# Optimization experiments

Measured on AMD Instinct MI355X. Metric: run time of the kernel, lower is better.

Reference implementation:

```python
import jax, jax.numpy as jnp
import numpy as np

N_NODES = 100000

def gcn_conv(x, row, col, w, W, b, n):
    # PyG GCNConv with edge weights: add self-loops, symmetric normalization.
    loop = jnp.arange(n)
    r = jnp.concatenate([row, loop])
    c = jnp.concatenate([col, loop])
    ew = jnp.concatenate([w, jnp.ones((n,), dtype=x.dtype)])
    deg = jax.ops.segment_sum(ew, c, num_segments=n)          # [N]
    dinv = jnp.where(deg > 0, jax.lax.rsqrt(deg), 0.0)
    norm = dinv[r] * ew * dinv[c]                              # [E+N]
    h = x @ W                                                  # [N, C]
    msg = norm[:, None] * h[r]                                 # [E+N, C]
    out = jax.ops.segment_sum(msg, c, num_segments=n)          # [N, C]
    return out + b

def setup_inputs() -> dict:
    key = jax.random.key(0)
    ks = jax.random.split(key, 9)
    n, F, H, O = N_NODES, 128, 128, 64  # H = 2*out_channels
    E = 1600000
    x = jax.random.normal(ks[0], (n, F), dtype=jnp.float32)
    edge_index = jax.random.randint(ks[1], (2, E), 0, n, dtype=jnp.int64)
    edge_attr = jax.random.uniform(ks[2], (E,), dtype=jnp.float32)
    s = 1.0 / np.sqrt(F)
    W1 = jax.random.uniform(ks[3], (F, H), jnp.float32, -s, s)
    b1 = jnp.zeros((H,), jnp.float32)
    s2 = 1.0 / np.sqrt(H)
    Wmu = jax.random.uniform(ks[4], (H, O), jnp.float32, -s2, s2)
    bmu = jnp.zeros((O,), jnp.float32)
    Wls = jax.random.uniform(ks[5], (H, O), jnp.float32, -s2, s2)
    bls = jnp.zeros((O,), jnp.float32)
    return {"x": x, "edge_index": edge_index, "edge_attr": edge_attr,
            "W1": W1, "b1": b1, "Wmu": Wmu, "bmu": bmu, "Wls": Wls, "bls": bls}

def reference(x, edge_index, edge_attr, W1, b1, Wmu, bmu, Wls, bls):
    n = x.shape[0]
    row, col = edge_index[0], edge_index[1]
    h = jax.nn.relu(gcn_conv(x, row, col, edge_attr, W1, b1, n))
    mu = gcn_conv(h, row, col, edge_attr, Wmu, bmu, n)
    logstd = gcn_conv(h, row, col, edge_attr, Wls, bls, n)
    return (mu, logstd)
```

## Files before the change

### kernel.cpp

```cpp
#include <hip/hip_runtime.h>
#include <math.h>


#define NBLK 1024

typedef __attribute__((ext_vector_type(8))) short bf16x8;
typedef __attribute__((ext_vector_type(4))) float f32x4;

__device__ __forceinline__ unsigned short f2bf_rne(float f) {
  unsigned int u = __float_as_uint(f);
  u += 0x7FFFu + ((u >> 16) & 1u);
  return (unsigned short)(u >> 16);
}

__device__ __forceinline__ float bf2f(unsigned short h) {
  return __uint_as_float(((unsigned int)h) << 16);
}

__device__ __forceinline__ unsigned int pack2(unsigned short a, unsigned short b) {
  return (unsigned int)a | ((unsigned int)b << 16);
}

__device__ __forceinline__ void lds_fadd(float* addr, float v) {
  unsigned int off = (unsigned int)(size_t)addr;
  asm volatile("ds_add_f32 %0, %1" : : "v"(off), "v"(v) : "memory");
}

__device__ __forceinline__ void ds_drain() {
  asm volatile("s_waitcnt lgkmcnt(0)" ::: "memory");
}


__global__ __launch_bounds__(256) void hist_coarse(const int* __restrict__ col,
                                                   int* __restrict__ G,
                                                   int E, int nbuck, int epb) {
  __shared__ int h[512];
  int blk = blockIdx.x;
  for (int i = threadIdx.x; i < nbuck; i += 256) h[i] = 0;
  __syncthreads();
  int beg = blk * epb;
  int end = min(beg + epb, E);
  for (int p = beg + threadIdx.x; p < end; p += 256)
    atomicAdd(&h[col[p] >> 8], 1);
  __syncthreads();
  for (int i = threadIdx.x; i < nbuck; i += 256)
    G[(size_t)i * NBLK + blk] = h[i];
}

__global__ __launch_bounds__(1024) void scan_bucket(int* __restrict__ G,
                                                    int* __restrict__ tot) {
  __shared__ int s[NBLK];
  int b = blockIdx.x;
  int v = G[(size_t)b * NBLK + threadIdx.x];
  s[threadIdx.x] = v;
  __syncthreads();
  for (int off = 1; off < NBLK; off <<= 1) {
    int t = (threadIdx.x >= off) ? s[threadIdx.x - off] : 0;
    __syncthreads();
    s[threadIdx.x] += t;
    __syncthreads();
  }
  G[(size_t)b * NBLK + threadIdx.x] = s[threadIdx.x] - v;
  if (threadIdx.x == NBLK - 1) tot[b] = s[NBLK - 1];
}

__global__ __launch_bounds__(512) void scan_start(const int* __restrict__ tot,
                                                  int* __restrict__ start,
                                                  int* __restrict__ row_ptr,
                                                  int nbuck, int N, int E) {
  __shared__ int s[512];
  int v = (threadIdx.x < nbuck) ? tot[threadIdx.x] : 0;
  s[threadIdx.x] = v;
  __syncthreads();
  for (int off = 1; off < 512; off <<= 1) {
    int t = (threadIdx.x >= off) ? s[threadIdx.x - off] : 0;
    __syncthreads();
    s[threadIdx.x] += t;
    __syncthreads();
  }
  if (threadIdx.x < nbuck) start[threadIdx.x] = s[threadIdx.x] - v;
  if (threadIdx.x == 511) start[nbuck] = E;
  if (threadIdx.x == 0) row_ptr[N] = E;
}

__global__ __launch_bounds__(256) void partition_edges(
    const int* __restrict__ row, const int* __restrict__ col,
    const float* __restrict__ w, const int* __restrict__ G,
    const int* __restrict__ start, int2* __restrict__ part,
    int E, int nbuck, int epb) {
  __shared__ int cur[512];
  int blk = blockIdx.x;
  for (int i = threadIdx.x; i < nbuck; i += 256)
    cur[i] = start[i] + G[(size_t)i * NBLK + blk];
  __syncthreads();
  int beg = blk * epb;
  int end = min(beg + epb, E);
  for (int p = beg + threadIdx.x; p < end; p += 256) {
    int c = col[p];
    int pos = atomicAdd(&cur[c >> 8], 1);
    part[pos] = make_int2(row[p] | ((c & 255) << 17),
                          __float_as_int(w[p]));
  }
}

__global__ __launch_bounds__(256) void build_fine(const int* __restrict__ start,
                                                  const int2* __restrict__ part,
                                                  int* __restrict__ row_ptr,
                                                  int2* __restrict__ csr,
                                                  float* __restrict__ dinv,
                                                  int N) {
  __shared__ int hist[256];
  __shared__ int sc[256];
  __shared__ int cur[256];
  __shared__ float deg[256];
  int b = blockIdx.x;
  int ebeg = start[b], eend = start[b + 1];
  hist[threadIdx.x] = 0;
  deg[threadIdx.x] = 0.f;
  __syncthreads();
  for (int p = ebeg + threadIdx.x; p < eend; p += 256) {
    int2 e = part[p];
    int dl = (e.x >> 17) & 255;
    atomicAdd(&hist[dl], 1);
    lds_fadd(&deg[dl], __int_as_float(e.y));
  }
  ds_drain();
  __syncthreads();
  int v = hist[threadIdx.x];
  sc[threadIdx.x] = v;
  __syncthreads();
  for (int off = 1; off < 256; off <<= 1) {
    int t = (threadIdx.x >= off) ? sc[threadIdx.x - off] : 0;
    __syncthreads();
    sc[threadIdx.x] += t;
    __syncthreads();
  }
  int ex = sc[threadIdx.x] - v;
  int node = b * 256 + threadIdx.x;
  if (node < N) {
    row_ptr[node] = ebeg + ex;
    dinv[node] = 1.0f / sqrtf(1.0f + deg[threadIdx.x]);
  }
  cur[threadIdx.x] = ebeg + ex;
  __syncthreads();
  for (int p = ebeg + threadIdx.x; p < eend; p += 256) {
    int2 r = part[p];
    int pos = atomicAdd(&cur[(r.x >> 17) & 255], 1);
    csr[pos] = make_int2(r.x & 0x1FFFF, r.y);
  }
}

__global__ void prep_wt(const float* __restrict__ Wsrc,
                        unsigned short* __restrict__ wt_hi,
                        unsigned short* __restrict__ wt_lo) {
  int i = blockIdx.x * blockDim.x + threadIdx.x;
  if (i >= 128 * 128) return;
  int n = i & 127, k = i >> 7;
  float f = Wsrc[(size_t)k * 128 + n];
  unsigned short h = f2bf_rne(f);
  unsigned short l = f2bf_rne(f - bf2f(h));
  wt_hi[(size_t)n * 128 + k] = h;
  wt_lo[(size_t)n * 128 + k] = l;
}

__global__ void prep_wcat_t(const float* __restrict__ Wmu, const float* __restrict__ Wls,
                            const float* __restrict__ bmu, const float* __restrict__ bls,
                            unsigned short* __restrict__ wt_hi,
                            unsigned short* __restrict__ wt_lo,
                            float* __restrict__ bcat) {
  int i = blockIdx.x * blockDim.x + threadIdx.x;
  if (i >= 128 * 128) return;
  int n = i & 127, k = i >> 7;
  float f = (n < 64) ? Wmu[(size_t)k * 64 + n] : Wls[(size_t)k * 64 + (n - 64)];
  unsigned short h = f2bf_rne(f);
  unsigned short l = f2bf_rne(f - bf2f(h));
  wt_hi[(size_t)n * 128 + k] = h;
  wt_lo[(size_t)n * 128 + k] = l;
  if (i < 128) bcat[i] = (i < 64) ? bmu[i] : bls[i - 64];
}

__global__ __launch_bounds__(256) void gemm_mfma(
    const float* __restrict__ A,
    const unsigned short* __restrict__ WtHi, const unsigned short* __restrict__ WtLo,
    const float* __restrict__ bias, const float* __restrict__ rowscale,
    float* __restrict__ C0, float* __restrict__ C1,
    unsigned short* __restrict__ Cbf, int split, int M) {
  __shared__ uint4 sAhi[1024];
  __shared__ uint4 sAlo[1024];
  __shared__ uint4 sWhi[1024];
  __shared__ uint4 sWlo[1024];

  int tid = threadIdx.x;
  int lane = tid & 63, wid = tid >> 6;
  int wave_r = (wid >> 1) * 64, wave_c = (wid & 1) * 64;
  int lrow = lane & 15, lkb = lane >> 4;
  int rowBase = blockIdx.x * 128;

  f32x4 acc[4][4];
#pragma unroll
  for (int mr = 0; mr < 4; ++mr)
#pragma unroll
    for (int nc = 0; nc < 4; ++nc) acc[mr][nc] = (f32x4){0.f, 0.f, 0.f, 0.f};

  const uint4* WtHi4 = (const uint4*)WtHi;
  const uint4* WtLo4 = (const uint4*)WtLo;

  for (int kt = 0; kt < 128; kt += 64) {
    __syncthreads();
#pragma unroll
    for (int j = 0; j < 4; ++j) {
      int g = tid + 256 * j;
      int c = g >> 3, k8 = g & 7;
      int slot = k8 ^ (c & 7);
      sWhi[c * 8 + slot] = WtHi4[c * 16 + (kt >> 3) + k8];
      sWlo[c * 8 + slot] = WtLo4[c * 16 + (kt >> 3) + k8];
    }
#pragma unroll
    for (int j = 0; j < 4; ++j) {
      int g = tid + 256 * j;
      int r = g >> 3, k8 = g & 7;
      int grow = rowBase + r;
      float4 v0 = make_float4(0.f, 0.f, 0.f, 0.f);
      float4 v1 = v0;
      if (grow < M) {
        const float4* Ar = (const float4*)(A + (size_t)grow * 128 + kt);
        v0 = Ar[k8 * 2];
        v1 = Ar[k8 * 2 + 1];
      }
      float f[8] = {v0.x, v0.y, v0.z, v0.w, v1.x, v1.y, v1.z, v1.w};
      unsigned short h[8], l[8];
#pragma unroll
      for (int q = 0; q < 8; ++q) {
        h[q] = f2bf_rne(f[q]);
        l[q] = f2bf_rne(f[q] - bf2f(h[q]));
      }
      int slot = k8 ^ (r & 7);
      sAhi[r * 8 + slot] = make_uint4(pack2(h[0], h[1]), pack2(h[2], h[3]),
                                      pack2(h[4], h[5]), pack2(h[6], h[7]));
      sAlo[r * 8 + slot] = make_uint4(pack2(l[0], l[1]), pack2(l[2], l[3]),
                                      pack2(l[4], l[5]), pack2(l[6], l[7]));
    }
    __syncthreads();
#pragma unroll
    for (int ks = 0; ks < 2; ++ks) {
      bf16x8 ah[4], al[4], bh[4], bl[4];
#pragma unroll
      for (int mr = 0; mr < 4; ++mr) {
        int r = wave_r + mr * 16 + lrow;
        int slot = (ks * 4 + lkb) ^ (r & 7);
        ah[mr] = *(const bf16x8*)&sAhi[r * 8 + slot];
        al[mr] = *(const bf16x8*)&sAlo[r * 8 + slot];
      }
#pragma unroll
      for (int nc = 0; nc < 4; ++nc) {
        int c = wave_c + nc * 16 + lrow;
        int slot = (ks * 4 + lkb) ^ (c & 7);
        bh[nc] = *(const bf16x8*)&sWhi[c * 8 + slot];
        bl[nc] = *(const bf16x8*)&sWlo[c * 8 + slot];
      }
#pragma unroll
      for (int mr = 0; mr < 4; ++mr)
#pragma unroll
        for (int nc = 0; nc < 4; ++nc) {
          acc[mr][nc] = __builtin_amdgcn_mfma_f32_16x16x32_bf16(
              ah[mr], bh[nc], acc[mr][nc], 0, 0, 0);
          acc[mr][nc] = __builtin_amdgcn_mfma_f32_16x16x32_bf16(
              al[mr], bh[nc], acc[mr][nc], 0, 0, 0);
          acc[mr][nc] = __builtin_amdgcn_mfma_f32_16x16x32_bf16(
              ah[mr], bl[nc], acc[mr][nc], 0, 0, 0);
        }
    }
  }

#pragma unroll
  for (int mr = 0; mr < 4; ++mr) {
    int Rb = rowBase + wave_r + mr * 16 + lkb * 4;
    float sc[4];
#pragma unroll
    for (int reg = 0; reg < 4; ++reg)
      sc[reg] = (rowscale && (Rb + reg) < M) ? rowscale[Rb + reg] : 1.0f;
#pragma unroll
    for (int nc = 0; nc < 4; ++nc) {
      int c = wave_c + nc * 16 + lrow;
      float bb = bias ? bias[c] : 0.f;
      f32x4 v = acc[mr][nc];
#pragma unroll
      for (int reg = 0; reg < 4; ++reg) {
        int R = Rb + reg;
        if (R >= M) continue;
        float val = v[reg] * sc[reg] + bb;
        if (Cbf) Cbf[(size_t)R * 128 + c] = f2bf_rne(val);
        if (C0) {
          if (c < split) C0[(size_t)R * split + c] = val;
          else           C1[(size_t)R * split + (c - split)] = val;
        }
      }
    }
  }
}

__global__ __launch_bounds__(256) void aggregate(
    const ushort4* __restrict__ hin, const int* __restrict__ row_ptr,
    const int2* __restrict__ csr, const float* __restrict__ dinv,
    const float4* __restrict__ bias4, ushort4* __restrict__ hout_bf,
    float4* __restrict__ hout_f4, int n, int do_relu, int scale_out) {
  int node = blockIdx.x * 8 + (threadIdx.x >> 5);
  if (node >= n) return;
  int t = threadIdx.x & 31;
  int beg = row_ptr[node], end = row_ptr[node + 1];
  ushort4 hs = hin[(size_t)node * 32 + t];
  float4 acc = make_float4(bf2f(hs.x), bf2f(hs.y), bf2f(hs.z), bf2f(hs.w));
  int p = beg;
  for (; p + 4 <= end; p += 4) {
    int2 e0 = csr[p + 0];
    int2 e1 = csr[p + 1];
    int2 e2 = csr[p + 2];
    int2 e3 = csr[p + 3];
    ushort4 h0 = hin[(size_t)e0.x * 32 + t];
    ushort4 h1 = hin[(size_t)e1.x * 32 + t];
    ushort4 h2 = hin[(size_t)e2.x * 32 + t];
    ushort4 h3 = hin[(size_t)e3.x * 32 + t];
    float w0 = __int_as_float(e0.y), w1 = __int_as_float(e1.y);
    float w2 = __int_as_float(e2.y), w3 = __int_as_float(e3.y);
    acc.x = fmaf(w0, bf2f(h0.x), acc.x); acc.y = fmaf(w0, bf2f(h0.y), acc.y);
    acc.z = fmaf(w0, bf2f(h0.z), acc.z); acc.w = fmaf(w0, bf2f(h0.w), acc.w);
    acc.x = fmaf(w1, bf2f(h1.x), acc.x); acc.y = fmaf(w1, bf2f(h1.y), acc.y);
    acc.z = fmaf(w1, bf2f(h1.z), acc.z); acc.w = fmaf(w1, bf2f(h1.w), acc.w);
    acc.x = fmaf(w2, bf2f(h2.x), acc.x); acc.y = fmaf(w2, bf2f(h2.y), acc.y);
    acc.z = fmaf(w2, bf2f(h2.z), acc.z); acc.w = fmaf(w2, bf2f(h2.w), acc.w);
    acc.x = fmaf(w3, bf2f(h3.x), acc.x); acc.y = fmaf(w3, bf2f(h3.y), acc.y);
    acc.z = fmaf(w3, bf2f(h3.z), acc.z); acc.w = fmaf(w3, bf2f(h3.w), acc.w);
  }
  for (; p < end; ++p) {
    int2 e = csr[p];
    ushort4 hv = hin[(size_t)e.x * 32 + t];
    float wv = __int_as_float(e.y);
    acc.x = fmaf(wv, bf2f(hv.x), acc.x); acc.y = fmaf(wv, bf2f(hv.y), acc.y);
    acc.z = fmaf(wv, bf2f(hv.z), acc.z); acc.w = fmaf(wv, bf2f(hv.w), acc.w);
  }
  float dc = dinv[node];
  float4 val = make_float4(dc * acc.x, dc * acc.y, dc * acc.z, dc * acc.w);
  if (bias4) {
    float4 b = bias4[t];
    val.x += b.x; val.y += b.y; val.z += b.z; val.w += b.w;
  }
  if (do_relu) {
    val.x = fmaxf(val.x, 0.f); val.y = fmaxf(val.y, 0.f);
    val.z = fmaxf(val.z, 0.f); val.w = fmaxf(val.w, 0.f);
  }
  if (scale_out) {
    val.x *= dc; val.y *= dc; val.z *= dc; val.w *= dc;
  }
  size_t o = (size_t)node * 32 + t;
  if (hout_bf) {
    ushort4 ov;
    ov.x = f2bf_rne(val.x); ov.y = f2bf_rne(val.y);
    ov.z = f2bf_rne(val.z); ov.w = f2bf_rne(val.w);
    hout_bf[o] = ov;
  }
  if (hout_f4) hout_f4[o] = val;
}

extern "C" void kernel_launch(void* const* d_in, const int* in_sizes, int n_in,
                              void* d_out, int out_size, void* d_ws, size_t ws_size,
                              hipStream_t stream) {
  const float* x   = (const float*)d_in[0];
  const int*   ei  = (const int*)d_in[1];
  const float* ea  = (const float*)d_in[2];
  const float* W1  = (const float*)d_in[3];
  const float* b1  = (const float*)d_in[4];
  const float* Wmu = (const float*)d_in[5];
  const float* bmu = (const float*)d_in[6];
  const float* Wls = (const float*)d_in[7];
  const float* bls = (const float*)d_in[8];
  const int N = in_sizes[0] / 128;
  const int E = in_sizes[2];
  const int* row = ei;
  const int* col = ei + E;

  char* p = (char*)d_ws;
  auto alloc = [&](size_t bytes) -> void* {
    void* r = (void*)p;
    p += (bytes + 255) & ~(size_t)255;
    return r;
  };
  float* dinv    = (float*)alloc((size_t)N * 4);
  int*   row_ptr = (int*)alloc((size_t)(N + 1) * 4);
  int*   start   = (int*)alloc(520 * 4);
  unsigned short* w1t_hi = (unsigned short*)alloc(128 * 128 * 2);
  unsigned short* w1t_lo = (unsigned short*)alloc(128 * 128 * 2);
  unsigned short* wct_hi = (unsigned short*)alloc(128 * 128 * 2);
  unsigned short* wct_lo = (unsigned short*)alloc(128 * 128 * 2);
  float* bcat    = (float*)alloc(128 * 4);
  int2*  csr     = (int2*)alloc((size_t)E * 8);
  float* bufA    = (float*)alloc((size_t)N * 128 * 4);
  unsigned short* bufB = (unsigned short*)alloc((size_t)N * 128 * 2);
  unsigned short* bufC = (unsigned short*)alloc((size_t)N * 128 * 2);

  const int nbuck = (N + 255) >> 8;
  const int epb   = (E + NBLK - 1) / NBLK;

  int2* part = (int2*)bufA;
  int*  G    = (int*)bufB;
  int*  tot  = (int*)((char*)bufB + (size_t)nbuck * NBLK * 4);

  float* out_mu = (float*)d_out;
  float* out_ls = out_mu + (size_t)N * 64;

  prep_wt<<<64, 256, 0, stream>>>(W1, w1t_hi, w1t_lo);
  prep_wcat_t<<<64, 256, 0, stream>>>(Wmu, Wls, bmu, bls, wct_hi, wct_lo, bcat);

  hist_coarse<<<NBLK, 256, 0, stream>>>(col, G, E, nbuck, epb);
  scan_bucket<<<nbuck, NBLK, 0, stream>>>(G, tot);
  scan_start<<<1, 512, 0, stream>>>(tot, start, row_ptr, nbuck, N, E);
  partition_edges<<<NBLK, 256, 0, stream>>>(row, col, ea, G, start, part,
                                            E, nbuck, epb);
  build_fine<<<nbuck, 256, 0, stream>>>(start, part, row_ptr, csr, dinv, N);

  int gblocks = (N + 127) / 128;
  int ablocks = (N + 7) / 8;
  gemm_mfma<<<gblocks, 256, 0, stream>>>(x, w1t_hi, w1t_lo, nullptr, dinv,
                                         nullptr, nullptr, bufB, 128, N);
  aggregate<<<ablocks, 256, 0, stream>>>((const ushort4*)bufB, row_ptr, csr, dinv,
                                         (const float4*)b1, (ushort4*)bufC,
                                         nullptr, N, 1, 1);
  aggregate<<<ablocks, 256, 0, stream>>>((const ushort4*)bufC, row_ptr, csr, dinv,
                                         nullptr, nullptr, (float4*)bufA, N, 0, 0);
  gemm_mfma<<<gblocks, 256, 0, stream>>>(bufA, wct_hi, wct_lo, bcat, nullptr,
                                         out_mu, out_ls, nullptr, 64, N);
}
```

Before: 280.9 us.

## Precompute bf16 hi/lo split in aggregate, merge weight prep, halve partition blocks

The second aggregate now writes its output as bf16 hi/lo pairs, and the final GEMM loads those pairs directly instead of reading fp32 and splitting it in-kernel. The total bytes moved are the same, but the split arithmetic shifts out of the GEMM load path. The two weight-prep kernels are merged into one launch. NBLK is halved to 512, which changes the number of histogram/partition blocks and the scan width, trading less parallelism for a smaller scan.

```diff
diff --git a/kernel.cpp b/kernel.cpp
--- a/kernel.cpp
+++ b/kernel.cpp
@@ -2,7 +2,7 @@
 #include <math.h>
 
 
-#define NBLK 1024
+#define NBLK 512
 
 typedef __attribute__((ext_vector_type(8))) short bf16x8;
 typedef __attribute__((ext_vector_type(4))) float f32x4;
@@ -47,7 +47,7 @@
     G[(size_t)i * NBLK + blk] = h[i];
 }
 
-__global__ __launch_bounds__(1024) void scan_bucket(int* __restrict__ G,
+__global__ __launch_bounds__(NBLK) void scan_bucket(int* __restrict__ G,
                                                     int* __restrict__ tot) {
   __shared__ int s[NBLK];
   int b = blockIdx.x;
@@ -150,37 +150,36 @@
   }
 }
 
-__global__ void prep_wt(const float* __restrict__ Wsrc,
-                        unsigned short* __restrict__ wt_hi,
-                        unsigned short* __restrict__ wt_lo) {
-  int i = blockIdx.x * blockDim.x + threadIdx.x;
-  if (i >= 128 * 128) return;
-  int n = i & 127, k = i >> 7;
-  float f = Wsrc[(size_t)k * 128 + n];
-  unsigned short h = f2bf_rne(f);
-  unsigned short l = f2bf_rne(f - bf2f(h));
-  wt_hi[(size_t)n * 128 + k] = h;
-  wt_lo[(size_t)n * 128 + k] = l;
-}
-
-__global__ void prep_wcat_t(const float* __restrict__ Wmu, const float* __restrict__ Wls,
-                            const float* __restrict__ bmu, const float* __restrict__ bls,
-                            unsigned short* __restrict__ wt_hi,
-                            unsigned short* __restrict__ wt_lo,
-                            float* __restrict__ bcat) {
-  int i = blockIdx.x * blockDim.x + threadIdx.x;
-  if (i >= 128 * 128) return;
-  int n = i & 127, k = i >> 7;
-  float f = (n < 64) ? Wmu[(size_t)k * 64 + n] : Wls[(size_t)k * 64 + (n - 64)];
-  unsigned short h = f2bf_rne(f);
-  unsigned short l = f2bf_rne(f - bf2f(h));
-  wt_hi[(size_t)n * 128 + k] = h;
-  wt_lo[(size_t)n * 128 + k] = l;
-  if (i < 128) bcat[i] = (i < 64) ? bmu[i] : bls[i - 64];
+__global__ __launch_bounds__(256) void prep_weights(
+    const float* __restrict__ W1,
+    const float* __restrict__ Wmu, const float* __restrict__ Wls,
+    const float* __restrict__ bmu, const float* __restrict__ bls,
+    unsigned short* __restrict__ w1t_hi, unsigned short* __restrict__ w1t_lo,
+    unsigned short* __restrict__ wct_hi, unsigned short* __restrict__ wct_lo,
+    float* __restrict__ bcat) {
+  int i = blockIdx.x * 256 + threadIdx.x;
+  if (i < 16384) {
+    int n = i & 127, k = i >> 7;
+    float f = W1[(size_t)k * 128 + n];
+    unsigned short h = f2bf_rne(f);
+    unsigned short l = f2bf_rne(f - bf2f(h));
+    w1t_hi[(size_t)n * 128 + k] = h;
+    w1t_lo[(size_t)n * 128 + k] = l;
+  } else {
+    int j = i - 16384;
+    int n = j & 127, k = j >> 7;
+    float f = (n < 64) ? Wmu[(size_t)k * 64 + n] : Wls[(size_t)k * 64 + (n - 64)];
+    unsigned short h = f2bf_rne(f);
+    unsigned short l = f2bf_rne(f - bf2f(h));
+    wct_hi[(size_t)n * 128 + k] = h;
+    wct_lo[(size_t)n * 128 + k] = l;
+    if (j < 128) bcat[j] = (j < 64) ? bmu[j] : bls[j - 64];
+  }
 }
 
 __global__ __launch_bounds__(256) void gemm_mfma(
     const float* __restrict__ A,
+    const unsigned short* __restrict__ AHi, const unsigned short* __restrict__ ALo,
     const unsigned short* __restrict__ WtHi, const unsigned short* __restrict__ WtLo,
     const float* __restrict__ bias, const float* __restrict__ rowscale,
     float* __restrict__ C0, float* __restrict__ C1,
@@ -204,6 +203,8 @@
 
   const uint4* WtHi4 = (const uint4*)WtHi;
   const uint4* WtLo4 = (const uint4*)WtLo;
+  const uint4* AHi4 = (const uint4*)AHi;
+  const uint4* ALo4 = (const uint4*)ALo;
 
   for (int kt = 0; kt < 128; kt += 64) {
     __syncthreads();
@@ -215,30 +216,48 @@
       sWhi[c * 8 + slot] = WtHi4[c * 16 + (kt >> 3) + k8];
       sWlo[c * 8 + slot] = WtLo4[c * 16 + (kt >> 3) + k8];
     }
-#pragma unroll
-    for (int j = 0; j < 4; ++j) {
-      int g = tid + 256 * j;
-      int r = g >> 3, k8 = g & 7;
-      int grow = rowBase + r;
-      float4 v0 = make_float4(0.f, 0.f, 0.f, 0.f);
-      float4 v1 = v0;
-      if (grow < M) {
-        const float4* Ar = (const float4*)(A + (size_t)grow * 128 + kt);
-        v0 = Ar[k8 * 2];
-        v1 = Ar[k8 * 2 + 1];
+    if (AHi) {
+#pragma unroll
+      for (int j = 0; j < 4; ++j) {
+        int g = tid + 256 * j;
+        int r = g >> 3, k8 = g & 7;
+        int grow = rowBase + r;
+        uint4 vh = make_uint4(0u, 0u, 0u, 0u);
+        uint4 vl = vh;
+        if (grow < M) {
+          vh = AHi4[(size_t)grow * 16 + (kt >> 3) + k8];
+          vl = ALo4[(size_t)grow * 16 + (kt >> 3) + k8];
+        }
+        int slot = k8 ^ (r & 7);
+        sAhi[r * 8 + slot] = vh;
+        sAlo[r * 8 + slot] = vl;
       }
-      float f[8] = {v0.x, v0.y, v0.z, v0.w, v1.x, v1.y, v1.z, v1.w};
-      unsigned short h[8], l[8];
-#pragma unroll
-      for (int q = 0; q < 8; ++q) {
-        h[q] = f2bf_rne(f[q]);
-        l[q] = f2bf_rne(f[q] - bf2f(h[q]));
+    } else {
+#pragma unroll
+      for (int j = 0; j < 4; ++j) {
+        int g = tid + 256 * j;
+        int r = g >> 3, k8 = g & 7;
+        int grow = rowBase + r;
+        float4 v0 = make_float4(0.f, 0.f, 0.f, 0.f);
+        float4 v1 = v0;
+        if (grow < M) {
+          const float4* Ar = (const float4*)(A + (size_t)grow * 128 + kt);
+          v0 = Ar[k8 * 2];
+          v1 = Ar[k8 * 2 + 1];
+        }
+        float f[8] = {v0.x, v0.y, v0.z, v0.w, v1.x, v1.y, v1.z, v1.w};
+        unsigned short h[8], l[8];
+#pragma unroll
+        for (int q = 0; q < 8; ++q) {
+          h[q] = f2bf_rne(f[q]);
+          l[q] = f2bf_rne(f[q] - bf2f(h[q]));
+        }
+        int slot = k8 ^ (r & 7);
+        sAhi[r * 8 + slot] = make_uint4(pack2(h[0], h[1]), pack2(h[2], h[3]),
+                                        pack2(h[4], h[5]), pack2(h[6], h[7]));
+        sAlo[r * 8 + slot] = make_uint4(pack2(l[0], l[1]), pack2(l[2], l[3]),
+                                        pack2(l[4], l[5]), pack2(l[6], l[7]));
       }
-      int slot = k8 ^ (r & 7);
-      sAhi[r * 8 + slot] = make_uint4(pack2(h[0], h[1]), pack2(h[2], h[3]),
-                                      pack2(h[4], h[5]), pack2(h[6], h[7]));
-      sAlo[r * 8 + slot] = make_uint4(pack2(l[0], l[1]), pack2(l[2], l[3]),
-                                      pack2(l[4], l[5]), pack2(l[6], l[7]));
     }
     __syncthreads();
 #pragma unroll
@@ -303,7 +322,8 @@
     const ushort4* __restrict__ hin, const int* __restrict__ row_ptr,
     const int2* __restrict__ csr, const float* __restrict__ dinv,
     const float4* __restrict__ bias4, ushort4* __restrict__ hout_bf,
-    float4* __restrict__ hout_f4, int n, int do_relu, int scale_out) {
+    ushort4* __restrict__ hout_hi, ushort4* __restrict__ hout_lo,
+    int n, int do_relu, int scale_out) {
   int node = blockIdx.x * 8 + (threadIdx.x >> 5);
   if (node >= n) return;
   int t = threadIdx.x & 31;
@@ -358,7 +378,15 @@
     ov.z = f2bf_rne(val.z); ov.w = f2bf_rne(val.w);
     hout_bf[o] = ov;
   }
-  if (hout_f4) hout_f4[o] = val;
+  if (hout_hi) {
+    ushort4 hv, lv;
+    hv.x = f2bf_rne(val.x); lv.x = f2bf_rne(val.x - bf2f(hv.x));
+    hv.y = f2bf_rne(val.y); lv.y = f2bf_rne(val.y - bf2f(hv.y));
+    hv.z = f2bf_rne(val.z); lv.z = f2bf_rne(val.z - bf2f(hv.z));
+    hv.w = f2bf_rne(val.w); lv.w = f2bf_rne(val.w - bf2f(hv.w));
+    hout_hi[o] = hv;
+    hout_lo[o] = lv;
+  }
 }
 
 extern "C" void kernel_launch(void* const* d_in, const int* in_sizes, int n_in,
@@ -393,22 +421,23 @@
   unsigned short* wct_lo = (unsigned short*)alloc(128 * 128 * 2);
   float* bcat    = (float*)alloc(128 * 4);
   int2*  csr     = (int2*)alloc((size_t)E * 8);
-  float* bufA    = (float*)alloc((size_t)N * 128 * 4);
+  unsigned short* bufAhi = (unsigned short*)alloc((size_t)N * 128 * 2);
+  unsigned short* bufAlo = (unsigned short*)alloc((size_t)N * 128 * 2);
   unsigned short* bufB = (unsigned short*)alloc((size_t)N * 128 * 2);
   unsigned short* bufC = (unsigned short*)alloc((size_t)N * 128 * 2);
 
   const int nbuck = (N + 255) >> 8;
   const int epb   = (E + NBLK - 1) / NBLK;
 
-  int2* part = (int2*)bufA;
+  int2* part = (int2*)bufAhi;
   int*  G    = (int*)bufB;
   int*  tot  = (int*)((char*)bufB + (size_t)nbuck * NBLK * 4);
 
   float* out_mu = (float*)d_out;
   float* out_ls = out_mu + (size_t)N * 64;
 
-  prep_wt<<<64, 256, 0, stream>>>(W1, w1t_hi, w1t_lo);
-  prep_wcat_t<<<64, 256, 0, stream>>>(Wmu, Wls, bmu, bls, wct_hi, wct_lo, bcat);
+  prep_weights<<<128, 256, 0, stream>>>(W1, Wmu, Wls, bmu, bls,
+                                        w1t_hi, w1t_lo, wct_hi, wct_lo, bcat);
 
   hist_coarse<<<NBLK, 256, 0, stream>>>(col, G, E, nbuck, epb);
   scan_bucket<<<nbuck, NBLK, 0, stream>>>(G, tot);
@@ -419,13 +448,16 @@
 
   int gblocks = (N + 127) / 128;
   int ablocks = (N + 7) / 8;
-  gemm_mfma<<<gblocks, 256, 0, stream>>>(x, w1t_hi, w1t_lo, nullptr, dinv,
-                                         nullptr, nullptr, bufB, 128, N);
+  gemm_mfma<<<gblocks, 256, 0, stream>>>(x, nullptr, nullptr, w1t_hi, w1t_lo,
+                                         nullptr, dinv, nullptr, nullptr,
+                                         bufB, 128, N);
   aggregate<<<ablocks, 256, 0, stream>>>((const ushort4*)bufB, row_ptr, csr, dinv,
                                          (const float4*)b1, (ushort4*)bufC,
-                                         nullptr, N, 1, 1);
+                                         nullptr, nullptr, N, 1, 1);
   aggregate<<<ablocks, 256, 0, stream>>>((const ushort4*)bufC, row_ptr, csr, dinv,
-                                         nullptr, nullptr, (float4*)bufA, N, 0, 0);
-  gemm_mfma<<<gblocks, 256, 0, stream>>>(bufA, wct_hi, wct_lo, bcat, nullptr,
-                                         out_mu, out_ls, nullptr, 64, N);
-}
+                                         nullptr, nullptr, (ushort4*)bufAhi,
+                                         (ushort4*)bufAlo, N, 0, 0);
+  gemm_mfma<<<gblocks, 256, 0, stream>>>(nullptr, bufAhi, bufAlo, wct_hi, wct_lo,
+                                         bcat, nullptr, out_mu, out_ls,
+                                         nullptr, 64, N);
+}
```

Result: faster. 272.1 us (-3.2%).
